# Kernel optimization log

Hardware: AMD Instinct MI355X
Metric: run time of the kernel (lower is better)

The kernel has to match this reference:

```python
import jax, jax.numpy as jnp
import numpy as np


def setup_inputs() -> dict:
    key = jax.random.key(0)
    k1, k2, k3, k4, k5 = jax.random.split(key, 5)
    B, S, D, H, L = 32, 2048, 512, 32, 2
    inp = jax.random.normal(k1, (B, S, D), dtype=jnp.float32)
    mask = jax.random.randint(k2, (B, S), 0, 2) > 0  # bool [B,S]
    projector = jax.random.normal(k3, (D, H), dtype=jnp.float32) * 0.05
    hidden = jax.random.normal(k4, (L - 1, H, H), dtype=jnp.float32) * 0.05
    evaluator = jax.random.normal(k5, (H, 1), dtype=jnp.float32) * 0.05
    return {"inp": inp, "mask": mask, "projector": projector,
            "hidden": hidden, "evaluator": evaluator}


def reference(inp, mask, projector, hidden, evaluator):
    act = jax.nn.sigmoid
    scale = jnp.asarray(projector.shape[-1], inp.dtype) ** 0.5  # sqrt(hidden_dim)
    m = mask.astype(inp.dtype)[..., None]          # [B,S,1]
    x = inp * m                                     # masked inputs (inp *= mask)
    w = act(jnp.einsum('bsd,dh->bsh', x, projector) / scale)
    for i in range(hidden.shape[0]):                # n_layers - 1 hidden matmuls
        w = act(jnp.einsum('bsh,hk->bsk', w, hidden[i]) / scale)
    w = act(jnp.einsum('bsh,ho->bso', w, evaluator) / scale)  # [B,S,1]
    w = jax.nn.softmax(w, axis=-2)                  # softmax over sequence axis
    w = w * m
    w = w / (jnp.sum(w, axis=1, keepdims=True) + 1e-12)
    return jnp.sum(w * x, axis=1)                   # [B,D]
```

## Files before the change

kernel.cpp:

```cpp
#include <hip/hip_runtime.h>

#define B_   32
#define S_   2048
#define D_   512
#define H_   32
#define BS_  (B_*S_)
#define NTILE_ (BS_/32)
#define TPB_   4
#define GRID_  (NTILE_/TPB_)
#define INV_SCALE 0.17677669529663689f


typedef short  s16x8 __attribute__((ext_vector_type(8)));
typedef float  f32x4 __attribute__((ext_vector_type(4)));

__device__ __forceinline__ float sigmoidf_(float x) {
    return 1.0f / (1.0f + __expf(-x));
}

__device__ __forceinline__ unsigned short f2bf(float f) {
    unsigned u = __float_as_uint(f);
    u += 0x7fffu + ((u >> 16) & 1u);
    return (unsigned short)(u >> 16);
}

__device__ __forceinline__ void barrier_lds() {
    asm volatile("s_waitcnt lgkmcnt(0)" ::: "memory");
    __builtin_amdgcn_s_barrier();
    asm volatile("" ::: "memory");
}

__global__ void kTransposeBf(const float* __restrict__ P, unsigned short* __restrict__ PTbf) {
    int o = blockIdx.x * 256 + threadIdx.x;
    int j = o >> 9, d = o & 511;
    PTbf[o] = f2bf(P[d * H_ + j]);
}

#define XST 520
#define WST 36

__global__ __launch_bounds__(256, 2) void kFused(
        const float* __restrict__ inp, const int* __restrict__ mask,
        const unsigned short* __restrict__ PTbf, const float* __restrict__ hd,
        const float* __restrict__ ev,
        float* __restrict__ partial, float2* __restrict__ zdm) {
    __shared__ __align__(16) unsigned short xs[32 * XST];
    __shared__ __align__(16) float w0f[32 * WST];
    __shared__ float cs[32];
    __shared__ float es[32];
    __shared__ float mskAll[TPB_ * 32];

    const int tid = threadIdx.x;
    const int wave = tid >> 6, lane = tid & 63;
    const int rt = wave & 1, ct = wave >> 1;
    const int m = lane & 15, quad = lane >> 4;
    const int tile0 = blockIdx.x * TPB_;

    s16x8 bf[16];
    {
        const unsigned short* brow = PTbf + (size_t)(ct * 16 + m) * 512 + quad * 8;
        #pragma unroll
        for (int ks = 0; ks < 16; ++ks)
            bf[ks] = *(const s16x8*)(brow + ks * 32);
    }
    const int k = tid & 31, slot = tid >> 5;
    float hdv[32];
    #pragma unroll
    for (int j = 0; j < 32; ++j) hdv[j] = hd[j * 32 + k];
    const float evk = ev[k];
    if (tid < TPB_ * 32)
        mskAll[tid] = (mask[tile0 * 32 + tid] != 0) ? 1.0f : 0.0f;

    float4 tmp[16];
    {
        const float4* g = (const float4*)inp + (size_t)tile0 * 4096;
        #pragma unroll
        for (int i = 0; i < 16; ++i)
            tmp[i] = g[i * 256 + tid];
    }

    for (int t = 0; t < TPB_; ++t) {
        const int tile = tile0 + t;

        #pragma unroll
        for (int i = 0; i < 16; ++i) {
            int fi = i * 256 + tid;
            int row = fi >> 7, kq = fi & 127;
            unsigned p0, p1;
            asm("v_cvt_pk_bf16_f32 %0, %1, %2" : "=v"(p0) : "v"(tmp[i].x), "v"(tmp[i].y));
            asm("v_cvt_pk_bf16_f32 %0, %1, %2" : "=v"(p1) : "v"(tmp[i].z), "v"(tmp[i].w));
            uint2 u; u.x = p0; u.y = p1;
            *(uint2*)(xs + row * XST + kq * 4) = u;
        }
        barrier_lds();

        if (t + 1 < TPB_) {
            const float4* g2 = (const float4*)inp + (size_t)(tile + 1) * 4096;
            #pragma unroll
            for (int i = 0; i < 16; ++i)
                tmp[i] = g2[i * 256 + tid];
        }

        const unsigned short* arow = xs + (rt * 16 + m) * XST + quad * 8;
        f32x4 acc = {0.f, 0.f, 0.f, 0.f};
        #pragma unroll
        for (int ks = 0; ks < 16; ++ks) {
            s16x8 a = *(const s16x8*)(arow + ks * 32);
            acc = __builtin_amdgcn_mfma_f32_16x16x32_bf16(a, bf[ks], acc, 0, 0, 0);
        }

        #pragma unroll
        for (int r = 0; r < 4; ++r) {
            int rowL = rt * 16 + quad * 4 + r;
            w0f[rowL * WST + ct * 16 + m] =
                sigmoidf_(mskAll[t * 32 + rowL] * acc[r] * INV_SCALE);
        }
        barrier_lds();

        #pragma unroll
        for (int tt = 0; tt < 4; ++tt) {
            const int row = slot + 8 * tt;
            const float4* wr = (const float4*)(w0f + row * WST);
            float s = 0.f;
            #pragma unroll
            for (int i = 0; i < 8; ++i) {
                float4 w4 = wr[i];
                s = fmaf(w4.x, hdv[4 * i + 0], s);
                s = fmaf(w4.y, hdv[4 * i + 1], s);
                s = fmaf(w4.z, hdv[4 * i + 2], s);
                s = fmaf(w4.w, hdv[4 * i + 3], s);
            }
            float val = sigmoidf_(s * INV_SCALE) * evk;
            #pragma unroll
            for (int o = 1; o < 32; o <<= 1)
                val += __shfl_xor(val, o);
            if (k == 0) {
                float v2 = sigmoidf_(val * INV_SCALE);
                float e  = __expf(v2);
                es[row] = e;
                cs[row] = mskAll[t * 32 + row] * e;
            }
        }
        barrier_lds();

        if (tid < 64) {
            float z = 0.f, dm = 0.f;
            if (tid < 32) { z = es[tid]; dm = cs[tid]; }
            #pragma unroll
            for (int o = 32; o > 0; o >>= 1) {
                z  += __shfl_down(z, o);
                dm += __shfl_down(dm, o);
            }
            if (tid == 0) zdm[tile] = make_float2(z, dm);
        }

        float a0 = 0.f, a1 = 0.f;
        #pragma unroll 8
        for (int row = 0; row < 32; ++row) {
            unsigned u = *(const unsigned*)(xs + row * XST + 2 * tid);
            float x0 = __uint_as_float(u << 16);
            float x1 = __uint_as_float(u & 0xffff0000u);
            float c = cs[row];
            a0 = fmaf(c, x0, a0);
            a1 = fmaf(c, x1, a1);
        }
        ((float2*)(partial + (size_t)tile * 512))[tid] = make_float2(a0, a1);

        barrier_lds();
    }
}

__global__ __launch_bounds__(1024) void kReduce(
        const float* __restrict__ partial, const float2* __restrict__ zdm,
        float* __restrict__ out) {
    const int b = blockIdx.x, tid = threadIdx.x;
    const int d2 = tid & 255;
    const int g  = tid >> 8;
    __shared__ float sInv;
    __shared__ float2 red[3][256];

    if (tid < 64) {
        float2 p = zdm[b * 64 + tid];
        float z = p.x, dm = p.y;
        #pragma unroll
        for (int o = 32; o > 0; o >>= 1) {
            z  += __shfl_down(z, o);
            dm += __shfl_down(dm, o);
        }
        if (tid == 0) sInv = 1.0f / (dm + 1e-12f * z);
    }

    const float2* pp = (const float2*)partial + (size_t)b * 64 * 256 + d2;
    float2 v[16];
    #pragma unroll
    for (int j = 0; j < 16; ++j)
        v[j] = pp[(size_t)(g * 16 + j) * 256];
    float a = 0.f, c = 0.f;
    #pragma unroll
    for (int j = 0; j < 16; ++j) { a += v[j].x; c += v[j].y; }

    if (g) red[g - 1][d2] = make_float2(a, c);
    __syncthreads();
    if (g == 0) {
        #pragma unroll
        for (int q = 0; q < 3; ++q) { a += red[q][d2].x; c += red[q][d2].y; }
        const float inv = sInv;
        ((float2*)out)[b * 256 + d2] = make_float2(a * inv, c * inv);
    }
}

extern "C" void kernel_launch(void* const* d_in, const int* in_sizes, int n_in,
                              void* d_out, int out_size, void* d_ws, size_t ws_size,
                              hipStream_t stream) {
    const float* inp  = (const float*)d_in[0];
    const int*   mask = (const int*)d_in[1];
    const float* proj = (const float*)d_in[2];
    const float* hid  = (const float*)d_in[3];
    const float* ev   = (const float*)d_in[4];
    float* out = (float*)d_out;

    unsigned short* PTbf = (unsigned short*)d_ws;
    float2* zdm     = (float2*)((char*)d_ws + 32768);
    float*  partial = (float*)((char*)d_ws + 49152);

    kTransposeBf<<<64, 256, 0, stream>>>(proj, PTbf);
    kFused      <<<GRID_, 256, 0, stream>>>(inp, mask, PTbf, hid, ev, partial, zdm);
    kReduce     <<<B_, 1024, 0, stream>>>(partial, zdm, out);
}
```

Baseline: 207.0 us.

## Raise fused-kernel occupancy by staging hidden weights in LDS and halving tiles per block

Tiles per block drop from 4 to 2, which doubles the grid, and the launch bounds now ask for 3 blocks per SM. The hidden-layer weights move from 32 per-thread registers into shared memory to free registers for that occupancy. The first input prefetch is issued before the B-fragment loads so it starts earlier. The reduction kernel is split into 8 chunks per batch with 256 threads each, giving more, smaller blocks. The trade-off is extra LDS reads in the hidden matmul and less prefetch overlap across tiles within each block.

```diff
diff --git a/kernel.cpp b/kernel.cpp
--- a/kernel.cpp
+++ b/kernel.cpp
@@ -6,7 +6,7 @@
 #define H_   32
 #define BS_  (B_*S_)
 #define NTILE_ (BS_/32)
-#define TPB_   4
+#define TPB_   2
 #define GRID_  (NTILE_/TPB_)
 #define INV_SCALE 0.17677669529663689f
 
@@ -39,13 +39,14 @@
 #define XST 520
 #define WST 36
 
-__global__ __launch_bounds__(256, 2) void kFused(
+__global__ __launch_bounds__(256, 3) void kFused(
         const float* __restrict__ inp, const int* __restrict__ mask,
         const unsigned short* __restrict__ PTbf, const float* __restrict__ hd,
         const float* __restrict__ ev,
         float* __restrict__ partial, float2* __restrict__ zdm) {
     __shared__ __align__(16) unsigned short xs[32 * XST];
     __shared__ __align__(16) float w0f[32 * WST];
+    __shared__ __align__(16) float hds[32 * 32];
     __shared__ float cs[32];
     __shared__ float es[32];
     __shared__ float mskAll[TPB_ * 32];
@@ -56,6 +57,14 @@
     const int m = lane & 15, quad = lane >> 4;
     const int tile0 = blockIdx.x * TPB_;
 
+    float4 tmp[16];
+    {
+        const float4* g = (const float4*)inp + (size_t)tile0 * 4096;
+        #pragma unroll
+        for (int i = 0; i < 16; ++i)
+            tmp[i] = g[i * 256 + tid];
+    }
+
     s16x8 bf[16];
     {
         const unsigned short* brow = PTbf + (size_t)(ct * 16 + m) * 512 + quad * 8;
@@ -64,20 +73,10 @@
             bf[ks] = *(const s16x8*)(brow + ks * 32);
     }
     const int k = tid & 31, slot = tid >> 5;
-    float hdv[32];
-    #pragma unroll
-    for (int j = 0; j < 32; ++j) hdv[j] = hd[j * 32 + k];
+    ((float4*)hds)[tid] = ((const float4*)hd)[tid];
     const float evk = ev[k];
     if (tid < TPB_ * 32)
         mskAll[tid] = (mask[tile0 * 32 + tid] != 0) ? 1.0f : 0.0f;
-
-    float4 tmp[16];
-    {
-        const float4* g = (const float4*)inp + (size_t)tile0 * 4096;
-        #pragma unroll
-        for (int i = 0; i < 16; ++i)
-            tmp[i] = g[i * 256 + tid];
-    }
 
     for (int t = 0; t < TPB_; ++t) {
         const int tile = tile0 + t;
@@ -125,10 +124,10 @@
             #pragma unroll
             for (int i = 0; i < 8; ++i) {
                 float4 w4 = wr[i];
-                s = fmaf(w4.x, hdv[4 * i + 0], s);
-                s = fmaf(w4.y, hdv[4 * i + 1], s);
-                s = fmaf(w4.z, hdv[4 * i + 2], s);
-                s = fmaf(w4.w, hdv[4 * i + 3], s);
+                s = fmaf(w4.x, hds[(4 * i + 0) * 32 + k], s);
+                s = fmaf(w4.y, hds[(4 * i + 1) * 32 + k], s);
+                s = fmaf(w4.z, hds[(4 * i + 2) * 32 + k], s);
+                s = fmaf(w4.w, hds[(4 * i + 3) * 32 + k], s);
             }
             float val = sigmoidf_(s * INV_SCALE) * evk;
             #pragma unroll
@@ -170,14 +169,16 @@
     }
 }
 
-__global__ __launch_bounds__(1024) void kReduce(
+__global__ __launch_bounds__(256) void kReduce(
         const float* __restrict__ partial, const float2* __restrict__ zdm,
         float* __restrict__ out) {
-    const int b = blockIdx.x, tid = threadIdx.x;
-    const int d2 = tid & 255;
-    const int g  = tid >> 8;
+    const int b = blockIdx.x >> 3, chunk = blockIdx.x & 7;
+    const int tid = threadIdx.x;
+    const int c  = tid & 31;
+    const int g  = tid >> 5;
+    const int d2 = chunk * 32 + c;
     __shared__ float sInv;
-    __shared__ float2 red[3][256];
+    __shared__ float2 red[7][32];
 
     if (tid < 64) {
         float2 p = zdm[b * 64 + tid];
@@ -191,21 +192,21 @@
     }
 
     const float2* pp = (const float2*)partial + (size_t)b * 64 * 256 + d2;
-    float2 v[16];
+    float2 v[8];
     #pragma unroll
-    for (int j = 0; j < 16; ++j)
-        v[j] = pp[(size_t)(g * 16 + j) * 256];
-    float a = 0.f, c = 0.f;
+    for (int j = 0; j < 8; ++j)
+        v[j] = pp[(size_t)(g * 8 + j) * 256];
+    float a = 0.f, cc = 0.f;
     #pragma unroll
-    for (int j = 0; j < 16; ++j) { a += v[j].x; c += v[j].y; }
-
-    if (g) red[g - 1][d2] = make_float2(a, c);
+    for (int j = 0; j < 8; ++j) { a += v[j].x; cc += v[j].y; }
+
+    if (g) red[g - 1][c] = make_float2(a, cc);
     __syncthreads();
     if (g == 0) {
         #pragma unroll
-        for (int q = 0; q < 3; ++q) { a += red[q][d2].x; c += red[q][d2].y; }
+        for (int q = 0; q < 7; ++q) { a += red[q][c].x; cc += red[q][c].y; }
         const float inv = sInv;
-        ((float2*)out)[b * 256 + d2] = make_float2(a * inv, c * inv);
+        ((float2*)out)[b * 256 + d2] = make_float2(a * inv, cc * inv);
     }
 }
 
@@ -225,5 +226,5 @@
 
     kTransposeBf<<<64, 256, 0, stream>>>(proj, PTbf);
     kFused      <<<GRID_, 256, 0, stream>>>(inp, mask, PTbf, hid, ev, partial, zdm);
-    kReduce     <<<B_, 1024, 0, stream>>>(partial, zdm, out);
-}
+    kReduce     <<<B_ * 8, 256, 0, stream>>>(partial, zdm, out);
+}
```

Result: slower. 259.8 us (+25.5%).

## Fuse projector transpose into main kernel and move hidden weights to LDS

Applied to the files above, without the earlier changes.

Drops the separate transpose/bf16-convert kernel and builds the MFMA B fragments inside the fused kernel, reading the projector directly and converting with packed bf16 instructions. Hidden-layer weights move from per-thread registers into shared memory to cut register pressure. The first input tile load is issued earlier, and the barrier now follows the next-tile prefetch. This removes one launch and the round trip of a workspace buffer, at the cost of strided projector loads per block and extra LDS reads in the hidden layer.

```diff
diff --git a/kernel.cpp b/kernel.cpp
--- a/kernel.cpp
+++ b/kernel.cpp
@@ -18,34 +18,23 @@
     return 1.0f / (1.0f + __expf(-x));
 }
 
-__device__ __forceinline__ unsigned short f2bf(float f) {
-    unsigned u = __float_as_uint(f);
-    u += 0x7fffu + ((u >> 16) & 1u);
-    return (unsigned short)(u >> 16);
-}
-
 __device__ __forceinline__ void barrier_lds() {
     asm volatile("s_waitcnt lgkmcnt(0)" ::: "memory");
     __builtin_amdgcn_s_barrier();
     asm volatile("" ::: "memory");
 }
 
-__global__ void kTransposeBf(const float* __restrict__ P, unsigned short* __restrict__ PTbf) {
-    int o = blockIdx.x * 256 + threadIdx.x;
-    int j = o >> 9, d = o & 511;
-    PTbf[o] = f2bf(P[d * H_ + j]);
-}
-
 #define XST 520
 #define WST 36
 
 __global__ __launch_bounds__(256, 2) void kFused(
         const float* __restrict__ inp, const int* __restrict__ mask,
-        const unsigned short* __restrict__ PTbf, const float* __restrict__ hd,
+        const float* __restrict__ proj, const float* __restrict__ hd,
         const float* __restrict__ ev,
         float* __restrict__ partial, float2* __restrict__ zdm) {
     __shared__ __align__(16) unsigned short xs[32 * XST];
     __shared__ __align__(16) float w0f[32 * WST];
+    __shared__ __align__(16) float hds[32 * 32];
     __shared__ float cs[32];
     __shared__ float es[32];
     __shared__ float mskAll[TPB_ * 32];
@@ -56,28 +45,41 @@
     const int m = lane & 15, quad = lane >> 4;
     const int tile0 = blockIdx.x * TPB_;
 
+    float4 tmp[16];
+    {
+        const float4* g = (const float4*)inp + (size_t)tile0 * 4096;
+        #pragma unroll
+        for (int i = 0; i < 16; ++i)
+            tmp[i] = g[i * 256 + tid];
+    }
+
     s16x8 bf[16];
     {
-        const unsigned short* brow = PTbf + (size_t)(ct * 16 + m) * 512 + quad * 8;
-        #pragma unroll
-        for (int ks = 0; ks < 16; ++ks)
-            bf[ks] = *(const s16x8*)(brow + ks * 32);
-    }
+        const int col = ct * 16 + m;
+        #pragma unroll
+        for (int ks = 0; ks < 16; ++ks) {
+            float f0 = proj[(size_t)(quad * 8 + ks * 32 + 0) * 32 + col];
+            float f1 = proj[(size_t)(quad * 8 + ks * 32 + 1) * 32 + col];
+            float f2 = proj[(size_t)(quad * 8 + ks * 32 + 2) * 32 + col];
+            float f3 = proj[(size_t)(quad * 8 + ks * 32 + 3) * 32 + col];
+            float f4 = proj[(size_t)(quad * 8 + ks * 32 + 4) * 32 + col];
+            float f5 = proj[(size_t)(quad * 8 + ks * 32 + 5) * 32 + col];
+            float f6 = proj[(size_t)(quad * 8 + ks * 32 + 6) * 32 + col];
+            float f7 = proj[(size_t)(quad * 8 + ks * 32 + 7) * 32 + col];
+            union { unsigned u[4]; s16x8 v; } bb;
+            asm("v_cvt_pk_bf16_f32 %0, %1, %2" : "=v"(bb.u[0]) : "v"(f0), "v"(f1));
+            asm("v_cvt_pk_bf16_f32 %0, %1, %2" : "=v"(bb.u[1]) : "v"(f2), "v"(f3));
+            asm("v_cvt_pk_bf16_f32 %0, %1, %2" : "=v"(bb.u[2]) : "v"(f4), "v"(f5));
+            asm("v_cvt_pk_bf16_f32 %0, %1, %2" : "=v"(bb.u[3]) : "v"(f6), "v"(f7));
+            bf[ks] = bb.v;
+        }
+    }
+
     const int k = tid & 31, slot = tid >> 5;
-    float hdv[32];
-    #pragma unroll
-    for (int j = 0; j < 32; ++j) hdv[j] = hd[j * 32 + k];
+    ((float4*)hds)[tid] = ((const float4*)hd)[tid];
     const float evk = ev[k];
     if (tid < TPB_ * 32)
         mskAll[tid] = (mask[tile0 * 32 + tid] != 0) ? 1.0f : 0.0f;
-
-    float4 tmp[16];
-    {
-        const float4* g = (const float4*)inp + (size_t)tile0 * 4096;
-        #pragma unroll
-        for (int i = 0; i < 16; ++i)
-            tmp[i] = g[i * 256 + tid];
-    }
 
     for (int t = 0; t < TPB_; ++t) {
         const int tile = tile0 + t;
@@ -92,7 +94,6 @@
             uint2 u; u.x = p0; u.y = p1;
             *(uint2*)(xs + row * XST + kq * 4) = u;
         }
-        barrier_lds();
 
         if (t + 1 < TPB_) {
             const float4* g2 = (const float4*)inp + (size_t)(tile + 1) * 4096;
@@ -100,6 +101,7 @@
             for (int i = 0; i < 16; ++i)
                 tmp[i] = g2[i * 256 + tid];
         }
+        barrier_lds();
 
         const unsigned short* arow = xs + (rt * 16 + m) * XST + quad * 8;
         f32x4 acc = {0.f, 0.f, 0.f, 0.f};
@@ -125,10 +127,10 @@
             #pragma unroll
             for (int i = 0; i < 8; ++i) {
                 float4 w4 = wr[i];
-                s = fmaf(w4.x, hdv[4 * i + 0], s);
-                s = fmaf(w4.y, hdv[4 * i + 1], s);
-                s = fmaf(w4.z, hdv[4 * i + 2], s);
-                s = fmaf(w4.w, hdv[4 * i + 3], s);
+                s = fmaf(w4.x, hds[(4 * i + 0) * 32 + k], s);
+                s = fmaf(w4.y, hds[(4 * i + 1) * 32 + k], s);
+                s = fmaf(w4.z, hds[(4 * i + 2) * 32 + k], s);
+                s = fmaf(w4.w, hds[(4 * i + 3) * 32 + k], s);
             }
             float val = sigmoidf_(s * INV_SCALE) * evk;
             #pragma unroll
@@ -219,11 +221,9 @@
     const float* ev   = (const float*)d_in[4];
     float* out = (float*)d_out;
 
-    unsigned short* PTbf = (unsigned short*)d_ws;
     float2* zdm     = (float2*)((char*)d_ws + 32768);
     float*  partial = (float*)((char*)d_ws + 49152);
 
-    kTransposeBf<<<64, 256, 0, stream>>>(proj, PTbf);
-    kFused      <<<GRID_, 256, 0, stream>>>(inp, mask, PTbf, hid, ev, partial, zdm);
-    kReduce     <<<B_, 1024, 0, stream>>>(partial, zdm, out);
-}
+    kFused <<<GRID_, 256, 0, stream>>>(inp, mask, proj, hid, ev, partial, zdm);
+    kReduce<<<B_, 1024, 0, stream>>>(partial, zdm, out);
+}
```

Measured after the change: 207.3 us. No clear change (+0.2%).
